# Kernel tuning notes

Measured on AMD Instinct MI355X. Metric: run time of the kernel, lower is better.

## Reference

```python
import jax, jax.numpy as jnp
import numpy as np

NEG_SLOPE = 0.2  # PyG GATConv default


def gat_layer(x, W, att_src, att_dst, bias, src, dst, concat):
    # x: [N, F_in]; W: [F_in, H*C]; att_src/att_dst: [H, C]; bias: [H*C] or [C]
    N = x.shape[0]
    H, C = att_src.shape
    h = (x @ W).reshape(N, H, C)                       # [N, H, C]
    a_s = jnp.einsum('nhc,hc->nh', h, att_src)         # [N, H]
    a_d = jnp.einsum('nhc,hc->nh', h, att_dst)
    e = jax.nn.leaky_relu(a_s[src] + a_d[dst], NEG_SLOPE)  # [E, H]
    # segment softmax over incoming edges of each destination node
    m = jax.ops.segment_max(e, dst, num_segments=N)
    m = jnp.where(jnp.isfinite(m), m, 0.0)
    ee = jnp.exp(e - m[dst])
    s = jax.ops.segment_sum(ee, dst, num_segments=N)
    alpha = ee / (s[dst] + 1e-16)                      # [E, H]
    out = jax.ops.segment_sum(h[src] * alpha[:, :, None], dst, num_segments=N)  # [N, H, C]
    out = out.reshape(N, H * C) if concat else out.mean(axis=1)
    return out + bias


def setup_inputs() -> dict:
    key = jax.random.key(0)
    ks = jax.random.split(key, 16)
    N, E, F_IN, NC = 100000, 3200000, 256, 40
    H, C = 8, 8  # hidden GATConv: heads=8, out=8 -> width 64
    inp = {}
    inp['features'] = jax.random.normal(ks[0], (N, F_IN), dtype=jnp.float32)
    inp['edge_index'] = jax.random.randint(ks[1], (2, E), 0, N, dtype=jnp.int64)
    def p(k, shape):
        return jax.random.normal(k, shape, dtype=jnp.float32) * 0.1
    # layer 0: in 256 -> 8 heads x 8 (concat -> 64)
    inp['W0'] = p(ks[2], (F_IN, H * C)); inp['as0'] = p(ks[3], (H, C)); inp['ad0'] = p(ks[4], (H, C)); inp['b0'] = jnp.zeros((H * C,), jnp.float32)
    # layer 1: 64 -> 8 heads x 8 (concat -> 64)
    inp['W1'] = p(ks[5], (H * C, H * C)); inp['as1'] = p(ks[6], (H, C)); inp['ad1'] = p(ks[7], (H, C)); inp['b1'] = jnp.zeros((H * C,), jnp.float32)
    # layer 2: 64 -> 1 head x n_classes (mean/no-concat)
    inp['W2'] = p(ks[8], (H * C, NC)); inp['as2'] = p(ks[9], (1, NC)); inp['ad2'] = p(ks[10], (1, NC)); inp['b2'] = jnp.zeros((NC,), jnp.float32)
    return inp


def reference(features, edge_index, W0, as0, ad0, b0, W1, as1, ad1, b1, W2, as2, ad2, b2):
    N = features.shape[0]
    loops = jnp.arange(N, dtype=edge_index.dtype)  # PyG GATConv adds self-loops by default
    src = jnp.concatenate([edge_index[0], loops])
    dst = jnp.concatenate([edge_index[1], loops])
    x = gat_layer(features, W0, as0, ad0, b0, src, dst, True)
    x = gat_layer(x, W1, as1, ad1, b1, src, dst, True)
    x = gat_layer(x, W2, as2, ad2, b2, src, dst, False)
    return jax.nn.log_softmax(x, axis=-1)
```

## Files before the change

kernel.cpp:

```cpp
#include <hip/hip_runtime.h>
#include <hip/hip_bf16.h>

#define NEG_SLOPE 0.2f
#define LOG2E 1.44269504f
#define EPB 8192
#define MAXBUCK 800

typedef __attribute__((ext_vector_type(8))) short short8;
typedef __attribute__((ext_vector_type(4))) float f32x4;

__device__ __forceinline__ unsigned short f2bf(float x) {
    unsigned u = __float_as_uint(x);
    unsigned r = (u + 0x7FFFu + ((u >> 16) & 1u)) >> 16;
    return (unsigned short)r;
}

__device__ __forceinline__ float fexp2(float x) {
    return __builtin_amdgcn_exp2f(x);
}

__device__ __forceinline__ float readlane_f(float v, int l) {
    return __int_as_float(__builtin_amdgcn_readlane(__float_as_int(v), l));
}


__global__ __launch_bounds__(256) void bucket_hist_k(
    const int* __restrict__ dsts, int* __restrict__ bcnt,
    int* __restrict__ bhist, int E, int nbuck) {
    __shared__ int lh[MAXBUCK];
    int t = threadIdx.x;
    for (int i = t; i < nbuck; i += 256) lh[i] = 0;
    __syncthreads();
    int base = blockIdx.x * EPB;
    int cnt = E - base;
    if (cnt > EPB) cnt = EPB;
    int nq = cnt >> 2;
    const int4* d4p = (const int4*)(dsts + base);
    for (int i = t; i < nq; i += 256) {
        int4 d = d4p[i];
        atomicAdd(&lh[d.x >> 7], 1);
        atomicAdd(&lh[d.y >> 7], 1);
        atomicAdd(&lh[d.z >> 7], 1);
        atomicAdd(&lh[d.w >> 7], 1);
    }
    for (int i = (nq << 2) + t; i < cnt; i += 256)
        atomicAdd(&lh[dsts[base + i] >> 7], 1);
    __syncthreads();
    int* bh = bhist + (size_t)blockIdx.x * MAXBUCK;
    for (int i = t; i < nbuck; i += 256) {
        int c = lh[i];
        bh[i] = c;
        if (c) atomicAdd(&bcnt[i], c);
    }
}

__global__ __launch_bounds__(512) void bucket_scan_k(
    const int* __restrict__ bcnt, int* __restrict__ bptrE,
    int* __restrict__ bcurE, int nbuck) {
    __shared__ int csum[512];
    int t = threadIdx.x;
    int i0 = t * 4;
    int v0 = 0, v1 = 0, v2 = 0, v3 = 0;
    if (i0 < nbuck) v0 = bcnt[i0];
    if (i0 + 1 < nbuck) v1 = bcnt[i0 + 1];
    if (i0 + 2 < nbuck) v2 = bcnt[i0 + 2];
    if (i0 + 3 < nbuck) v3 = bcnt[i0 + 3];
    int s = v0 + v1 + v2 + v3;
    csum[t] = s;
    __syncthreads();
    for (int off = 1; off < 512; off <<= 1) {
        int x = (t >= off) ? csum[t - off] : 0;
        __syncthreads();
        csum[t] += x;
        __syncthreads();
    }
    int base = csum[t] - s;
    if (i0 < nbuck)     { bptrE[i0] = base;     bcurE[i0] = base; }     base += v0;
    if (i0 + 1 < nbuck) { bptrE[i0 + 1] = base; bcurE[i0 + 1] = base; } base += v1;
    if (i0 + 2 < nbuck) { bptrE[i0 + 2] = base; bcurE[i0 + 2] = base; } base += v2;
    if (i0 + 3 < nbuck) { bptrE[i0 + 3] = base; bcurE[i0 + 3] = base; }
}

__global__ __launch_bounds__(256) void bscatter_k(
    const int* __restrict__ srcs, const int* __restrict__ dsts,
    const int* __restrict__ bhist, int* __restrict__ bcurE,
    int* __restrict__ pairs, int E, int nbuck) {
    __shared__ int lh[MAXBUCK];
    __shared__ int lbase[MAXBUCK];
    int t = threadIdx.x;
    const int* bh = bhist + (size_t)blockIdx.x * MAXBUCK;
    for (int i = t; i < nbuck; i += 256) {
        int c = bh[i];
        lbase[i] = c ? atomicAdd(&bcurE[i], c) : 0;
        lh[i] = 0;
    }
    __syncthreads();
    int base = blockIdx.x * EPB;
    int cnt = E - base;
    if (cnt > EPB) cnt = EPB;
    int nq = cnt >> 2;
    const int4* d4p = (const int4*)(dsts + base);
    const int4* s4p = (const int4*)(srcs + base);
    for (int i = t; i < nq; i += 256) {
        int4 d = d4p[i];
        int4 s = s4p[i];
        int b0 = d.x >> 7, b1 = d.y >> 7, b2 = d.z >> 7, b3 = d.w >> 7;
        int r0 = atomicAdd(&lh[b0], 1);
        int r1 = atomicAdd(&lh[b1], 1);
        int r2 = atomicAdd(&lh[b2], 1);
        int r3 = atomicAdd(&lh[b3], 1);
        pairs[lbase[b0] + r0] = (s.x << 7) | (d.x & 127);
        pairs[lbase[b1] + r1] = (s.y << 7) | (d.y & 127);
        pairs[lbase[b2] + r2] = (s.z << 7) | (d.z & 127);
        pairs[lbase[b3] + r3] = (s.w << 7) | (d.w & 127);
    }
    for (int i = (nq << 2) + t; i < cnt; i += 256) {
        int s = srcs[base + i], d = dsts[base + i];
        int r = atomicAdd(&lh[d >> 7], 1);
        pairs[lbase[d >> 7] + r] = (s << 7) | (d & 127);
    }
}

__global__ __launch_bounds__(256) void bucket_sort_k(
    const int* __restrict__ pairs, const int* __restrict__ bptrE,
    const int* __restrict__ bcurE, int* __restrict__ row_ptr,
    int* __restrict__ csr_src, int N, int Etot) {
    __shared__ int lh[128];
    __shared__ int sc[128];
    int b = blockIdx.x;
    int n0 = b << 7;
    int t = threadIdx.x;
    if (t < 128) lh[t] = 0;
    __syncthreads();
    int e0 = bptrE[b], e1 = bcurE[b];
    for (int e = e0 + t; e < e1; e += 256)
        atomicAdd(&lh[pairs[e] & 127], 1);
    __syncthreads();
    if (t < 128) sc[t] = lh[t];
    __syncthreads();
    for (int off = 1; off < 128; off <<= 1) {
        int x = (t < 128 && t >= off) ? sc[t - off] : 0;
        __syncthreads();
        if (t < 128) sc[t] += x;
        __syncthreads();
    }
    if (t < 128) {
        int cntv = lh[t];
        int excl = sc[t] - cntv;
        int n = n0 + t;
        int rp = e0 + n0 + t + excl;
        if (n < N) {
            row_ptr[n] = rp;
            csr_src[rp] = n;
        }
        lh[t] = rp + 1;
    }
    __syncthreads();
    for (int e = e0 + t; e < e1; e += 256) {
        int p = pairs[e];
        int pos = atomicAdd(&lh[p & 127], 1);
        csr_src[pos] = p >> 7;
    }
    if (b == 0 && t == 0) row_ptr[N] = Etot;
}


template <int K>
__global__ __launch_bounds__(256) void gemm_pack8_k(
    const float* __restrict__ x, const float* __restrict__ W,
    const float* __restrict__ a_src, const float* __restrict__ a_dst,
    char* __restrict__ hrec, float* __restrict__ asb,
    float* __restrict__ adb, int N) {
    constexpr int NT = 4;
    constexpr int KT = K / 32;
    constexpr size_t WF_BYTES = (size_t)KT * NT * 64 * 8 * sizeof(short);
    constexpr size_t H_BYTES = (size_t)64 * 65 * sizeof(float);
    __shared__ alignas(16) char smem[WF_BYTES > H_BYTES ? WF_BYTES : H_BYTES];
    short* Wf = (short*)smem;
    float* hL = (float*)smem;
    int tid = threadIdx.x;
    for (int f = tid; f < KT * NT * 64; f += 256) {
        int lane = f & 63;
        int ntk = f >> 6;
        int nt = ntk % NT, kt = ntk / NT;
        int q = lane >> 4, c = lane & 15;
        int n = nt * 16 + c;
        int k0 = kt * 32 + q * 8;
        short8 frag;
        #pragma unroll
        for (int j = 0; j < 8; ++j)
            frag[j] = (short)f2bf(W[(size_t)(k0 + j) * 64 + n]);
        *(short8*)&Wf[f * 8] = frag;
    }
    __syncthreads();
    int wave = tid >> 6, lane = tid & 63;
    int q = lane >> 4, c = lane & 15;
    int m0 = blockIdx.x * 64 + wave * 16;
    int arow = m0 + c;
    int arl = arow < N ? arow : N - 1;
    f32x4 acc[NT] = {};
    for (int kt = 0; kt < KT; ++kt) {
        const float* xp = x + (size_t)arl * K + kt * 32 + q * 8;
        float4 a0 = *(const float4*)xp;
        float4 a1 = *(const float4*)(xp + 4);
        float av[8] = {a0.x, a0.y, a0.z, a0.w, a1.x, a1.y, a1.z, a1.w};
        short8 af;
        #pragma unroll
        for (int j = 0; j < 8; ++j) af[j] = (short)f2bf(av[j]);
        #pragma unroll
        for (int nt = 0; nt < NT; ++nt) {
            short8 bf = *(const short8*)&Wf[((kt * NT + nt) * 64 + lane) * 8];
            acc[nt] = __builtin_amdgcn_mfma_f32_16x16x32_bf16(af, bf, acc[nt],
                                                              0, 0, 0);
        }
    }
    __syncthreads();
    int lrow = wave * 16 + q * 4;
    #pragma unroll
    for (int nt = 0; nt < NT; ++nt)
        #pragma unroll
        for (int reg = 0; reg < 4; ++reg)
            hL[(lrow + reg) * 65 + nt * 16 + c] = acc[nt][reg];
    __syncthreads();
    #pragma unroll
    for (int it = 0; it < 2; ++it) {
        int id = it * 256 + tid;
        int ln = id >> 3, hd = id & 7;
        int gn = blockIdx.x * 64 + ln;
        if (gn >= N) continue;
        const float* hp = &hL[ln * 65 + hd * 8];
        float as = 0.f, ad = 0.f;
        float hv[8];
        #pragma unroll
        for (int j = 0; j < 8; ++j) {
            hv[j] = hp[j];
            as += hv[j] * a_src[hd * 8 + j];
            ad += hv[j] * a_dst[hd * 8 + j];
        }
        adb[gn * 8 + hd] = ad * LOG2E;
        asb[gn * 8 + hd] = as * LOG2E;
        unsigned short u[8];
        #pragma unroll
        for (int j = 0; j < 8; ++j) u[j] = f2bf(hv[j]);
        uint4 pk;
        pk.x = (unsigned)u[0] | ((unsigned)u[1] << 16);
        pk.y = (unsigned)u[2] | ((unsigned)u[3] << 16);
        pk.z = (unsigned)u[4] | ((unsigned)u[5] << 16);
        pk.w = (unsigned)u[6] | ((unsigned)u[7] << 16);
        *(uint4*)(hrec + (size_t)gn * 128 + hd * 16) = pk;
    }
}


__global__ __launch_bounds__(256) void gemm_pack40_k(
    const float* __restrict__ x, const float* __restrict__ W,
    const float* __restrict__ a_src, const float* __restrict__ a_dst,
    char* __restrict__ h40, float* __restrict__ asb40,
    float* __restrict__ adb, int N) {
    constexpr int K = 64, NT = 3, KT = 2;
    constexpr size_t WF_BYTES = (size_t)KT * NT * 64 * 8 * sizeof(short);
    constexpr size_t H_BYTES = (size_t)64 * 41 * sizeof(float);
    __shared__ alignas(16) char smem[WF_BYTES > H_BYTES ? WF_BYTES : H_BYTES];
    short* Wf = (short*)smem;
    float* hL = (float*)smem;
    int tid = threadIdx.x;
    for (int f = tid; f < KT * NT * 64; f += 256) {
        int lane = f & 63;
        int ntk = f >> 6;
        int nt = ntk % NT, kt = ntk / NT;
        int q = lane >> 4, c = lane & 15;
        int n = nt * 16 + c;
        int k0 = kt * 32 + q * 8;
        short8 frag;
        #pragma unroll
        for (int j = 0; j < 8; ++j) {
            float v = (n < 40) ? W[(size_t)(k0 + j) * 40 + n] : 0.f;
            frag[j] = (short)f2bf(v);
        }
        *(short8*)&Wf[f * 8] = frag;
    }
    __syncthreads();
    int wave = tid >> 6, lane = tid & 63;
    int q = lane >> 4, c = lane & 15;
    int m0 = blockIdx.x * 64 + wave * 16;
    int arow = m0 + c;
    int arl = arow < N ? arow : N - 1;
    f32x4 acc[NT] = {};
    for (int kt = 0; kt < KT; ++kt) {
        const float* xp = x + (size_t)arl * K + kt * 32 + q * 8;
        float4 a0 = *(const float4*)xp;
        float4 a1 = *(const float4*)(xp + 4);
        float av[8] = {a0.x, a0.y, a0.z, a0.w, a1.x, a1.y, a1.z, a1.w};
        short8 af;
        #pragma unroll
        for (int j = 0; j < 8; ++j) af[j] = (short)f2bf(av[j]);
        #pragma unroll
        for (int nt = 0; nt < NT; ++nt) {
            short8 bf = *(const short8*)&Wf[((kt * NT + nt) * 64 + lane) * 8];
            acc[nt] = __builtin_amdgcn_mfma_f32_16x16x32_bf16(af, bf, acc[nt],
                                                              0, 0, 0);
        }
    }
    __syncthreads();
    int lrow = wave * 16 + q * 4;
    #pragma unroll
    for (int nt = 0; nt < NT; ++nt) {
        int n = nt * 16 + c;
        if (n >= 40) continue;
        #pragma unroll
        for (int reg = 0; reg < 4; ++reg)
            hL[(lrow + reg) * 41 + n] = acc[nt][reg];
    }
    __syncthreads();
    int ln = tid >> 2, sub = tid & 3;
    int gn = blockIdx.x * 64 + ln;
    float pas = 0.f, pad = 0.f;
    if (gn < N) {
        for (int j = sub; j < 40; j += 4) {
            float hv = hL[ln * 41 + j];
            pas += hv * a_src[j];
            pad += hv * a_dst[j];
        }
    }
    pas += __shfl_xor(pas, 1); pas += __shfl_xor(pas, 2);
    pad += __shfl_xor(pad, 1); pad += __shfl_xor(pad, 2);
    if (gn < N && sub == 0) {
        asb40[gn] = pas * LOG2E;
        adb[gn] = pad * LOG2E;
    }
    for (int i = tid; i < 64 * 40; i += 256) {
        int n2 = i / 40, ch = i % 40;
        int g2 = blockIdx.x * 64 + n2;
        if (g2 < N)
            *(unsigned short*)(h40 + (size_t)g2 * 80 + ch * 2) =
                f2bf(hL[n2 * 41 + ch]);
    }
}


#define EDGE64(SUF, IDX)                                                     \
    int s##SUF = __builtin_amdgcn_readlane(sv, (IDX));                       \
    float w##SUF = lwp[(IDX)];                                               \
    unsigned u##SUF =                                                        \
        *(const unsigned short*)(hrec + (size_t)s##SUF * 128 + lane2);

__global__ __launch_bounds__(256) void aggr64_k(
    const char* __restrict__ hrec, const float* __restrict__ asb,
    const float* __restrict__ adb, const int* __restrict__ row_ptr,
    const int* __restrict__ csr_src, const float* __restrict__ bias,
    float* __restrict__ out, int N) {
    __shared__ float wlds[4 * 1040];
    int wave = threadIdx.x >> 6;
    int node = blockIdx.x * 4 + wave;
    if (node >= N) return;
    int lane = threadIdx.x & 63;
    int hd = lane >> 3;
    int lane2 = lane * 2;
    float* wbA = wlds + wave * 1040;
    float* wbB = wbA + 520;
    const float* lwpA = wbA + hd * 65;
    const float* lwpB = wbB + hd * 65;
    int beg = row_ptr[node], end = row_ptr[node + 1];
    float4 adv0 = *(const float4*)(adb + (size_t)node * 8);
    float4 adv1 = *(const float4*)(adb + (size_t)node * 8 + 4);
    float acc0 = 0.f, acc1 = 0.f, acc2 = 0.f, acc3 = 0.f;
    float acc4 = 0.f, acc5 = 0.f, acc6 = 0.f, acc7 = 0.f;
    float l0 = 0.f, l1 = 0.f, l2 = 0.f, l3 = 0.f;
    float l4 = 0.f, l5 = 0.f, l6 = 0.f, l7 = 0.f;
    int par = 0;
    for (int i0 = beg; i0 < end; i0 += 64, par ^= 1) {
        int tail = end - i0;
        int sv = csr_src[i0 + (lane < tail ? lane : 0)];
        int cnt = tail < 64 ? tail : 64;
        float* wb = par ? wbB : wbA;
        const float* lwp = par ? lwpB : lwpA;
        {
            const float* asp = asb + (size_t)sv * 8;
            float4 s0 = *(const float4*)asp;
            float4 s1 = *(const float4*)(asp + 4);
            float w0 = s0.x + adv0.x; w0 = fmaxf(w0, NEG_SLOPE * w0); w0 = fexp2(w0);
            float w1 = s0.y + adv0.y; w1 = fmaxf(w1, NEG_SLOPE * w1); w1 = fexp2(w1);
            float w2 = s0.z + adv0.z; w2 = fmaxf(w2, NEG_SLOPE * w2); w2 = fexp2(w2);
            float w3 = s0.w + adv0.w; w3 = fmaxf(w3, NEG_SLOPE * w3); w3 = fexp2(w3);
            float w4 = s1.x + adv1.x; w4 = fmaxf(w4, NEG_SLOPE * w4); w4 = fexp2(w4);
            float w5 = s1.y + adv1.y; w5 = fmaxf(w5, NEG_SLOPE * w5); w5 = fexp2(w5);
            float w6 = s1.z + adv1.z; w6 = fmaxf(w6, NEG_SLOPE * w6); w6 = fexp2(w6);
            float w7 = s1.w + adv1.w; w7 = fmaxf(w7, NEG_SLOPE * w7); w7 = fexp2(w7);
            wb[lane]       = w0;
            wb[65 + lane]  = w1;
            wb[130 + lane] = w2;
            wb[195 + lane] = w3;
            wb[260 + lane] = w4;
            wb[325 + lane] = w5;
            wb[390 + lane] = w6;
            wb[455 + lane] = w7;
        }
        int j = 0;
        for (; j + 8 <= cnt; j += 8) {
            EDGE64(A, j)      EDGE64(B, j + 1) EDGE64(C, j + 2) EDGE64(D, j + 3)
            EDGE64(E2, j + 4) EDGE64(F, j + 5) EDGE64(G, j + 6) EDGE64(H2, j + 7)
            l0 += wA; l1 += wB; l2 += wC; l3 += wD;
            l4 += wE2; l5 += wF; l6 += wG; l7 += wH2;
            acc0 = fmaf(wA, __uint_as_float(uA << 16), acc0);
            acc1 = fmaf(wB, __uint_as_float(uB << 16), acc1);
            acc2 = fmaf(wC, __uint_as_float(uC << 16), acc2);
            acc3 = fmaf(wD, __uint_as_float(uD << 16), acc3);
            acc4 = fmaf(wE2, __uint_as_float(uE2 << 16), acc4);
            acc5 = fmaf(wF, __uint_as_float(uF << 16), acc5);
            acc6 = fmaf(wG, __uint_as_float(uG << 16), acc6);
            acc7 = fmaf(wH2, __uint_as_float(uH2 << 16), acc7);
        }
        for (; j + 4 <= cnt; j += 4) {
            EDGE64(A, j) EDGE64(B, j + 1) EDGE64(C, j + 2) EDGE64(D, j + 3)
            l0 += wA; l1 += wB; l2 += wC; l3 += wD;
            acc0 = fmaf(wA, __uint_as_float(uA << 16), acc0);
            acc1 = fmaf(wB, __uint_as_float(uB << 16), acc1);
            acc2 = fmaf(wC, __uint_as_float(uC << 16), acc2);
            acc3 = fmaf(wD, __uint_as_float(uD << 16), acc3);
        }
        for (; j < cnt; ++j) {
            EDGE64(A, j)
            l0 += wA;
            acc0 = fmaf(wA, __uint_as_float(uA << 16), acc0);
        }
    }
    float l = ((l0 + l1) + (l2 + l3)) + ((l4 + l5) + (l6 + l7));
    float acc = ((acc0 + acc1) + (acc2 + acc3)) + ((acc4 + acc5) + (acc6 + acc7));
    out[(size_t)node * 64 + lane] = acc / (l + 1e-16f) + bias[lane];
}


#define F40(SUF, IDX)                                                        \
    int s##SUF = __builtin_amdgcn_readlane(sv, (IDX));                       \
    float w##SUF = readlane_f(wv, (IDX));                                    \
    unsigned u##SUF =                                                        \
        *(const unsigned short*)(rec40 + (size_t)s##SUF * 80 + cl2);

__global__ __launch_bounds__(256) void aggr40_k(
    const char* __restrict__ rec40, const float* __restrict__ asb,
    const float* __restrict__ adb, const int* __restrict__ row_ptr,
    const int* __restrict__ csr_src, const float* __restrict__ bias,
    float* __restrict__ out, int N) {
    int node = blockIdx.x * 4 + (threadIdx.x >> 6);
    if (node >= N) return;
    int lane = threadIdx.x & 63;
    int cl2 = (lane < 40 ? lane : 0) * 2;
    int beg = row_ptr[node], end = row_ptr[node + 1];
    float ad = adb[node];
    float acc0 = 0.f, acc1 = 0.f, acc2 = 0.f, acc3 = 0.f;
    float acc4 = 0.f, acc5 = 0.f, acc6 = 0.f, acc7 = 0.f;
    float lpart = 0.f;
    for (int i0 = beg; i0 < end; i0 += 64) {
        int tail = end - i0;
        int sv = csr_src[i0 + (lane < tail ? lane : 0)];
        int cnt = tail < 64 ? tail : 64;
        float as = asb[sv];
        float v = as + ad;
        v = fmaxf(v, NEG_SLOPE * v);
        float wv = fexp2(v);
        wv = (lane < cnt) ? wv : 0.f;
        lpart += wv;
        int j = 0;
        for (; j + 8 <= cnt; j += 8) {
            F40(A, j)     F40(B, j + 1) F40(C, j + 2) F40(D, j + 3)
            F40(E2, j + 4) F40(F, j + 5) F40(G, j + 6) F40(H2, j + 7)
            acc0 = fmaf(wA, __uint_as_float(uA << 16), acc0);
            acc1 = fmaf(wB, __uint_as_float(uB << 16), acc1);
            acc2 = fmaf(wC, __uint_as_float(uC << 16), acc2);
            acc3 = fmaf(wD, __uint_as_float(uD << 16), acc3);
            acc4 = fmaf(wE2, __uint_as_float(uE2 << 16), acc4);
            acc5 = fmaf(wF, __uint_as_float(uF << 16), acc5);
            acc6 = fmaf(wG, __uint_as_float(uG << 16), acc6);
            acc7 = fmaf(wH2, __uint_as_float(uH2 << 16), acc7);
        }
        for (; j + 4 <= cnt; j += 4) {
            F40(A, j) F40(B, j + 1) F40(C, j + 2) F40(D, j + 3)
            acc0 = fmaf(wA, __uint_as_float(uA << 16), acc0);
            acc1 = fmaf(wB, __uint_as_float(uB << 16), acc1);
            acc2 = fmaf(wC, __uint_as_float(uC << 16), acc2);
            acc3 = fmaf(wD, __uint_as_float(uD << 16), acc3);
        }
        for (; j < cnt; ++j) {
            F40(A, j)
            acc0 = fmaf(wA, __uint_as_float(uA << 16), acc0);
        }
    }
    #pragma unroll
    for (int off = 32; off > 0; off >>= 1) lpart += __shfl_xor(lpart, off);
    float l = lpart;
    float acc = ((acc0 + acc1) + (acc2 + acc3)) + ((acc4 + acc5) + (acc6 + acc7));
    float val = acc / (l + 1e-16f) + ((lane < 40) ? bias[lane] : 0.f);
    float mval = (lane < 40) ? val : -1e30f;
    #pragma unroll
    for (int off = 32; off > 0; off >>= 1)
        mval = fmaxf(mval, __shfl_xor(mval, off));
    float ex = (lane < 40) ? __expf(val - mval) : 0.f;
    #pragma unroll
    for (int off = 32; off > 0; off >>= 1) ex += __shfl_xor(ex, off);
    if (lane < 40)
        out[(size_t)node * 40 + lane] = val - mval - __logf(ex);
}


extern "C" void kernel_launch(void* const* d_in, const int* in_sizes, int n_in,
                              void* d_out, int out_size, void* d_ws,
                              size_t ws_size, hipStream_t stream) {
    const float* features = (const float*)d_in[0];
    const int* edge_index = (const int*)d_in[1];
    const float* W0 = (const float*)d_in[2];
    const float* as0 = (const float*)d_in[3];
    const float* ad0 = (const float*)d_in[4];
    const float* b0 = (const float*)d_in[5];
    const float* W1 = (const float*)d_in[6];
    const float* as1 = (const float*)d_in[7];
    const float* ad1 = (const float*)d_in[8];
    const float* b1 = (const float*)d_in[9];
    const float* W2 = (const float*)d_in[10];
    const float* as2 = (const float*)d_in[11];
    const float* ad2 = (const float*)d_in[12];
    const float* b2 = (const float*)d_in[13];

    int N = in_sizes[0] / 256;
    int E = in_sizes[1] / 2;
    int Etot = E + N;
    int nbuck = (N + 127) >> 7;
    const int* srcs = edge_index;
    const int* dsts = edge_index + E;

    float* ws = (float*)d_ws;
    float* Hbuf = ws;
    float* Abuf = Hbuf + (size_t)N * 64;
    float* adb  = Abuf + (size_t)N * 64;
    float* asb  = adb + (size_t)N * 8;
    char* hrec  = (char*)(asb + (size_t)N * 8);
    int* row_ptr = (int*)(hrec + (size_t)N * 128);
    int* bcnt    = row_ptr + (N + 2);
    int* bptrE   = bcnt + MAXBUCK;
    int* bcurE   = bptrE + MAXBUCK;
    int* csr_src = bcurE + MAXBUCK;
    int* bhist   = csr_src + Etot;
    int* pairs   = (int*)Hbuf;

    const int B = 256;
    int gAg = (N + 3) / 4;
    int gGm = (N + 63) / 64;
    int gSc = (E + EPB - 1) / EPB;

    (void)hipMemsetAsync(bcnt, 0, MAXBUCK * 4, stream);
    bucket_hist_k<<<gSc, B, 0, stream>>>(dsts, bcnt, bhist, E, nbuck);
    bucket_scan_k<<<1, 512, 0, stream>>>(bcnt, bptrE, bcurE, nbuck);
    bscatter_k<<<gSc, B, 0, stream>>>(srcs, dsts, bhist, bcurE, pairs, E,
                                      nbuck);
    bucket_sort_k<<<nbuck, B, 0, stream>>>(pairs, bptrE, bcurE, row_ptr,
                                           csr_src, N, Etot);

    gemm_pack8_k<256><<<gGm, B, 0, stream>>>(features, W0, as0, ad0, hrec,
                                             asb, adb, N);
    aggr64_k<<<gAg, B, 0, stream>>>(hrec, asb, adb, row_ptr, csr_src, b0,
                                    Abuf, N);

    gemm_pack8_k<64><<<gGm, B, 0, stream>>>(Abuf, W1, as1, ad1, hrec, asb,
                                            adb, N);
    aggr64_k<<<gAg, B, 0, stream>>>(hrec, asb, adb, row_ptr, csr_src, b1,
                                    Abuf, N);

    gemm_pack40_k<<<gGm, B, 0, stream>>>(Abuf, W2, as2, ad2, hrec, asb, adb,
                                         N);
    aggr40_k<<<gAg, B, 0, stream>>>(hrec, asb, adb, row_ptr, csr_src, b2,
                                    (float*)d_out, N);
}
```

Before: 579.6 us.

## Store pre-scaled byte offsets in CSR, pad layer-3 records, simplify edge loops

The CSR source array now stores node index shifted by 7 (a 128-byte record offset), so the gather kernels skip the multiply when addressing. The layer-3 record goes from 80 to 128 bytes and holds the source attention score inside it, which removes a separate scattered load per edge. The 4-wide and scalar tail loops in both aggregation kernels are dropped: weights of lanes past the count are zeroed and the 8-wide loop always runs, which does extra gathers on partial chunks. The histogram and scatter kernels switch to 512-thread blocks. The shifted indices limit N to what fits in 25 bits, and reading asb via sv>>2 relies on the shift matching the 32-byte per-node stride.

```diff
diff --git a/kernel.cpp b/kernel.cpp
--- a/kernel.cpp
+++ b/kernel.cpp
@@ -24,30 +24,30 @@
 }
 
 
-__global__ __launch_bounds__(256) void bucket_hist_k(
+__global__ __launch_bounds__(512) void bucket_hist_k(
     const int* __restrict__ dsts, int* __restrict__ bcnt,
     int* __restrict__ bhist, int E, int nbuck) {
     __shared__ int lh[MAXBUCK];
     int t = threadIdx.x;
-    for (int i = t; i < nbuck; i += 256) lh[i] = 0;
+    for (int i = t; i < nbuck; i += 512) lh[i] = 0;
     __syncthreads();
     int base = blockIdx.x * EPB;
     int cnt = E - base;
     if (cnt > EPB) cnt = EPB;
     int nq = cnt >> 2;
     const int4* d4p = (const int4*)(dsts + base);
-    for (int i = t; i < nq; i += 256) {
+    for (int i = t; i < nq; i += 512) {
         int4 d = d4p[i];
         atomicAdd(&lh[d.x >> 7], 1);
         atomicAdd(&lh[d.y >> 7], 1);
         atomicAdd(&lh[d.z >> 7], 1);
         atomicAdd(&lh[d.w >> 7], 1);
     }
-    for (int i = (nq << 2) + t; i < cnt; i += 256)
+    for (int i = (nq << 2) + t; i < cnt; i += 512)
         atomicAdd(&lh[dsts[base + i] >> 7], 1);
     __syncthreads();
     int* bh = bhist + (size_t)blockIdx.x * MAXBUCK;
-    for (int i = t; i < nbuck; i += 256) {
+    for (int i = t; i < nbuck; i += 512) {
         int c = lh[i];
         bh[i] = c;
         if (c) atomicAdd(&bcnt[i], c);
@@ -81,7 +81,7 @@
     if (i0 + 3 < nbuck) { bptrE[i0 + 3] = base; bcurE[i0 + 3] = base; }
 }
 
-__global__ __launch_bounds__(256) void bscatter_k(
+__global__ __launch_bounds__(512) void bscatter_k(
     const int* __restrict__ srcs, const int* __restrict__ dsts,
     const int* __restrict__ bhist, int* __restrict__ bcurE,
     int* __restrict__ pairs, int E, int nbuck) {
@@ -89,7 +89,7 @@
     __shared__ int lbase[MAXBUCK];
     int t = threadIdx.x;
     const int* bh = bhist + (size_t)blockIdx.x * MAXBUCK;
-    for (int i = t; i < nbuck; i += 256) {
+    for (int i = t; i < nbuck; i += 512) {
         int c = bh[i];
         lbase[i] = c ? atomicAdd(&bcurE[i], c) : 0;
         lh[i] = 0;
@@ -101,7 +101,7 @@
     int nq = cnt >> 2;
     const int4* d4p = (const int4*)(dsts + base);
     const int4* s4p = (const int4*)(srcs + base);
-    for (int i = t; i < nq; i += 256) {
+    for (int i = t; i < nq; i += 512) {
         int4 d = d4p[i];
         int4 s = s4p[i];
         int b0 = d.x >> 7, b1 = d.y >> 7, b2 = d.z >> 7, b3 = d.w >> 7;
@@ -114,7 +114,7 @@
         pairs[lbase[b2] + r2] = (s.z << 7) | (d.z & 127);
         pairs[lbase[b3] + r3] = (s.w << 7) | (d.w & 127);
     }
-    for (int i = (nq << 2) + t; i < cnt; i += 256) {
+    for (int i = (nq << 2) + t; i < cnt; i += 512) {
         int s = srcs[base + i], d = dsts[base + i];
         int r = atomicAdd(&lh[d >> 7], 1);
         pairs[lbase[d >> 7] + r] = (s << 7) | (d & 127);
@@ -151,7 +151,7 @@
         int rp = e0 + n0 + t + excl;
         if (n < N) {
             row_ptr[n] = rp;
-            csr_src[rp] = n;
+            csr_src[rp] = n << 7;
         }
         lh[t] = rp + 1;
     }
@@ -159,7 +159,7 @@
     for (int e = e0 + t; e < e1; e += 256) {
         int p = pairs[e];
         int pos = atomicAdd(&lh[p & 127], 1);
-        csr_src[pos] = p >> 7;
+        csr_src[pos] = p & ~127;
     }
     if (b == 0 && t == 0) row_ptr[N] = Etot;
 }
@@ -255,8 +255,7 @@
 __global__ __launch_bounds__(256) void gemm_pack40_k(
     const float* __restrict__ x, const float* __restrict__ W,
     const float* __restrict__ a_src, const float* __restrict__ a_dst,
-    char* __restrict__ h40, float* __restrict__ asb40,
-    float* __restrict__ adb, int N) {
+    char* __restrict__ rec40, float* __restrict__ adb, int N) {
     constexpr int K = 64, NT = 3, KT = 2;
     constexpr size_t WF_BYTES = (size_t)KT * NT * 64 * 8 * sizeof(short);
     constexpr size_t H_BYTES = (size_t)64 * 41 * sizeof(float);
@@ -325,14 +324,14 @@
     pas += __shfl_xor(pas, 1); pas += __shfl_xor(pas, 2);
     pad += __shfl_xor(pad, 1); pad += __shfl_xor(pad, 2);
     if (gn < N && sub == 0) {
-        asb40[gn] = pas * LOG2E;
+        *(float*)(rec40 + (size_t)gn * 128 + 80) = pas * LOG2E;
         adb[gn] = pad * LOG2E;
     }
     for (int i = tid; i < 64 * 40; i += 256) {
         int n2 = i / 40, ch = i % 40;
         int g2 = blockIdx.x * 64 + n2;
         if (g2 < N)
-            *(unsigned short*)(h40 + (size_t)g2 * 80 + ch * 2) =
+            *(unsigned short*)(rec40 + (size_t)g2 * 128 + ch * 2) =
                 f2bf(hL[n2 * 41 + ch]);
     }
 }
@@ -342,7 +341,7 @@
     int s##SUF = __builtin_amdgcn_readlane(sv, (IDX));                       \
     float w##SUF = lwp[(IDX)];                                               \
     unsigned u##SUF =                                                        \
-        *(const unsigned short*)(hrec + (size_t)s##SUF * 128 + lane2);
+        *(const unsigned short*)(hrec + (size_t)(unsigned)s##SUF + lane2);
 
 __global__ __launch_bounds__(256) void aggr64_k(
     const char* __restrict__ hrec, const float* __restrict__ asb,
@@ -375,7 +374,8 @@
         float* wb = par ? wbB : wbA;
         const float* lwp = par ? lwpB : lwpA;
         {
-            const float* asp = asb + (size_t)sv * 8;
+            const float* asp =
+                (const float*)((const char*)asb + (((unsigned)sv) >> 2));
             float4 s0 = *(const float4*)asp;
             float4 s1 = *(const float4*)(asp + 4);
             float w0 = s0.x + adv0.x; w0 = fmaxf(w0, NEG_SLOPE * w0); w0 = fexp2(w0);
@@ -386,6 +386,10 @@
             float w5 = s1.y + adv1.y; w5 = fmaxf(w5, NEG_SLOPE * w5); w5 = fexp2(w5);
             float w6 = s1.z + adv1.z; w6 = fmaxf(w6, NEG_SLOPE * w6); w6 = fexp2(w6);
             float w7 = s1.w + adv1.w; w7 = fmaxf(w7, NEG_SLOPE * w7); w7 = fexp2(w7);
+            if (lane >= cnt) {
+                w0 = 0.f; w1 = 0.f; w2 = 0.f; w3 = 0.f;
+                w4 = 0.f; w5 = 0.f; w6 = 0.f; w7 = 0.f;
+            }
             wb[lane]       = w0;
             wb[65 + lane]  = w1;
             wb[130 + lane] = w2;
@@ -395,8 +399,7 @@
             wb[390 + lane] = w6;
             wb[455 + lane] = w7;
         }
-        int j = 0;
-        for (; j + 8 <= cnt; j += 8) {
+        for (int j = 0; j < cnt; j += 8) {
             EDGE64(A, j)      EDGE64(B, j + 1) EDGE64(C, j + 2) EDGE64(D, j + 3)
             EDGE64(E2, j + 4) EDGE64(F, j + 5) EDGE64(G, j + 6) EDGE64(H2, j + 7)
             l0 += wA; l1 += wB; l2 += wC; l3 += wD;
@@ -410,19 +413,6 @@
             acc6 = fmaf(wG, __uint_as_float(uG << 16), acc6);
             acc7 = fmaf(wH2, __uint_as_float(uH2 << 16), acc7);
         }
-        for (; j + 4 <= cnt; j += 4) {
-            EDGE64(A, j) EDGE64(B, j + 1) EDGE64(C, j + 2) EDGE64(D, j + 3)
-            l0 += wA; l1 += wB; l2 += wC; l3 += wD;
-            acc0 = fmaf(wA, __uint_as_float(uA << 16), acc0);
-            acc1 = fmaf(wB, __uint_as_float(uB << 16), acc1);
-            acc2 = fmaf(wC, __uint_as_float(uC << 16), acc2);
-            acc3 = fmaf(wD, __uint_as_float(uD << 16), acc3);
-        }
-        for (; j < cnt; ++j) {
-            EDGE64(A, j)
-            l0 += wA;
-            acc0 = fmaf(wA, __uint_as_float(uA << 16), acc0);
-        }
     }
     float l = ((l0 + l1) + (l2 + l3)) + ((l4 + l5) + (l6 + l7));
     float acc = ((acc0 + acc1) + (acc2 + acc3)) + ((acc4 + acc5) + (acc6 + acc7));
@@ -434,13 +424,12 @@
     int s##SUF = __builtin_amdgcn_readlane(sv, (IDX));                       \
     float w##SUF = readlane_f(wv, (IDX));                                    \
     unsigned u##SUF =                                                        \
-        *(const unsigned short*)(rec40 + (size_t)s##SUF * 80 + cl2);
+        *(const unsigned short*)(rec40 + (size_t)(unsigned)s##SUF + cl2);
 
 __global__ __launch_bounds__(256) void aggr40_k(
-    const char* __restrict__ rec40, const float* __restrict__ asb,
-    const float* __restrict__ adb, const int* __restrict__ row_ptr,
-    const int* __restrict__ csr_src, const float* __restrict__ bias,
-    float* __restrict__ out, int N) {
+    const char* __restrict__ rec40, const float* __restrict__ adb,
+    const int* __restrict__ row_ptr, const int* __restrict__ csr_src,
+    const float* __restrict__ bias, float* __restrict__ out, int N) {
     int node = blockIdx.x * 4 + (threadIdx.x >> 6);
     if (node >= N) return;
     int lane = threadIdx.x & 63;
@@ -454,14 +443,13 @@
         int tail = end - i0;
         int sv = csr_src[i0 + (lane < tail ? lane : 0)];
         int cnt = tail < 64 ? tail : 64;
-        float as = asb[sv];
+        float as = *(const float*)(rec40 + (size_t)(unsigned)sv + 80);
         float v = as + ad;
         v = fmaxf(v, NEG_SLOPE * v);
         float wv = fexp2(v);
         wv = (lane < cnt) ? wv : 0.f;
         lpart += wv;
-        int j = 0;
-        for (; j + 8 <= cnt; j += 8) {
+        for (int j = 0; j < cnt; j += 8) {
             F40(A, j)     F40(B, j + 1) F40(C, j + 2) F40(D, j + 3)
             F40(E2, j + 4) F40(F, j + 5) F40(G, j + 6) F40(H2, j + 7)
             acc0 = fmaf(wA, __uint_as_float(uA << 16), acc0);
@@ -472,17 +460,6 @@
             acc5 = fmaf(wF, __uint_as_float(uF << 16), acc5);
             acc6 = fmaf(wG, __uint_as_float(uG << 16), acc6);
             acc7 = fmaf(wH2, __uint_as_float(uH2 << 16), acc7);
-        }
-        for (; j + 4 <= cnt; j += 4) {
-            F40(A, j) F40(B, j + 1) F40(C, j + 2) F40(D, j + 3)
-            acc0 = fmaf(wA, __uint_as_float(uA << 16), acc0);
-            acc1 = fmaf(wB, __uint_as_float(uB << 16), acc1);
-            acc2 = fmaf(wC, __uint_as_float(uC << 16), acc2);
-            acc3 = fmaf(wD, __uint_as_float(uD << 16), acc3);
-        }
-        for (; j < cnt; ++j) {
-            F40(A, j)
-            acc0 = fmaf(wA, __uint_as_float(uA << 16), acc0);
         }
     }
     #pragma unroll
@@ -547,10 +524,10 @@
     int gSc = (E + EPB - 1) / EPB;
 
     (void)hipMemsetAsync(bcnt, 0, MAXBUCK * 4, stream);
-    bucket_hist_k<<<gSc, B, 0, stream>>>(dsts, bcnt, bhist, E, nbuck);
+    bucket_hist_k<<<gSc, 512, 0, stream>>>(dsts, bcnt, bhist, E, nbuck);
     bucket_scan_k<<<1, 512, 0, stream>>>(bcnt, bptrE, bcurE, nbuck);
-    bscatter_k<<<gSc, B, 0, stream>>>(srcs, dsts, bhist, bcurE, pairs, E,
-                                      nbuck);
+    bscatter_k<<<gSc, 512, 0, stream>>>(srcs, dsts, bhist, bcurE, pairs, E,
+                                        nbuck);
     bucket_sort_k<<<nbuck, B, 0, stream>>>(pairs, bptrE, bcurE, row_ptr,
                                            csr_src, N, Etot);
 
@@ -564,8 +541,7 @@
     aggr64_k<<<gAg, B, 0, stream>>>(hrec, asb, adb, row_ptr, csr_src, b1,
                                     Abuf, N);
 
-    gemm_pack40_k<<<gGm, B, 0, stream>>>(Abuf, W2, as2, ad2, hrec, asb, adb,
-                                         N);
-    aggr40_k<<<gAg, B, 0, stream>>>(hrec, asb, adb, row_ptr, csr_src, b2,
+    gemm_pack40_k<<<gGm, B, 0, stream>>>(Abuf, W2, as2, ad2, hrec, adb, N);
+    aggr40_k<<<gAg, B, 0, stream>>>(hrec, adb, row_ptr, csr_src, b2,
                                     (float*)d_out, N);
 }
```

Result: no change. 575.1 us (-0.8%).
